# Kernel tuning notes

Measured on AMD Instinct MI355X. Metric: run time of the kernel, lower is better.

The kernel has to match this reference:

```python
import jax, jax.numpy as jnp
import numpy as np

ACT_BITS = 8
W_BITS = 8
C_IN = 64


def round_ste(x):
    # straight-through rounding (Brevitas training behavior)
    return x + jax.lax.stop_gradient(jnp.round(x) - x)


def fake_quant(x, scale, bits, signed):
    if signed:
        lo, hi = -(2 ** (bits - 1)), 2 ** (bits - 1) - 1
    else:
        lo, hi = 0, 2 ** bits - 1
    return jnp.clip(round_ste(x / scale), lo, hi) * scale


def conv_nchw(x, w, pad, groups=1):
    return jax.lax.conv_general_dilated(
        x, w, window_strides=(1, 1), padding=((pad, pad), (pad, pad)),
        dimension_numbers=("NCHW", "OIHW", "NCHW"), feature_group_count=groups)


def setup_inputs() -> dict:
    key = jax.random.key(0)
    k0, k1, k2, k3 = jax.random.split(key, 4)
    x = jax.random.normal(k0, (8, 64, 112, 112), jnp.float32)
    w1 = jax.random.normal(k1, (64, 1, 3, 3), jnp.float32) * 0.05    # depthwise 3x3
    w2 = jax.random.normal(k2, (128, 64, 1, 1), jnp.float32) * 0.05  # pointwise 1x1
    w_sc = jax.random.normal(k3, (128, 64, 1, 1), jnp.float32) * 0.05  # shortcut 1x1
    sc = lambda v: jnp.asarray(v, jnp.float32)
    return dict(x=x, w1=w1, w2=w2, w_sc=w_sc,
                s_in=sc(0.03), s_relu=sc(0.02), s_add=sc(0.03),
                sw1=sc(0.004), sw2=sc(0.004), sw_sc=sc(0.004))


def reference(x, w1, w2, w_sc, s_in, s_relu, s_add, sw1, sw2, sw_sc):
    # quant_input: signed 8-bit fake-quant of the activation
    xq = fake_quant(x, s_in, ACT_BITS, True)
    # shortcut: 1x1 conv with int8 fake-quantized weights (inplane != ouplane)
    identity = conv_nchw(xq, fake_quant(w_sc, sw_sc, W_BITS, True), pad=0)
    # conv1: depthwise 3x3 (groups=inplane) with int8 fake-quantized weights
    y = conv_nchw(xq, fake_quant(w1, sw1, W_BITS, True), pad=1, groups=C_IN)
    # relu2: QuantReLU -> unsigned 8-bit fake-quant of relu
    y = fake_quant(jax.nn.relu(y), s_relu, ACT_BITS, False)
    # conv2: pointwise 1x1
    y = conv_nchw(y, fake_quant(w2, sw2, W_BITS, True), pad=0)
    # residual_add: add then requantize to signed 8-bit
    return fake_quant(y + identity, s_add, ACT_BITS, True)
```

## Files before the change

### kernel.cpp

```cpp
#include <hip/hip_runtime.h>
#include <hip/hip_bf16.h>
#include <stdint.h>

#define NIMG 8
#define CIN  64
#define HWI  12544
#define NP   100352
#define COUT 128

typedef short v8s __attribute__((ext_vector_type(8)));
typedef float v4f __attribute__((ext_vector_type(4)));

static __device__ __forceinline__ int q8(float x, float inv, float lo, float hi) {
    float t = rintf(x * inv);
    t = fminf(fmaxf(t, lo), hi);
    return (int)t;
}

static __device__ __forceinline__ uint32_t funnel(uint32_t hi, uint32_t lo, int sh) {
    return (uint32_t)(((((uint64_t)hi) << 32) | (uint64_t)lo) >> sh);
}

static __device__ __forceinline__ int dot4(uint32_t a, uint32_t b, int c) {
    int acc = c;
    #pragma unroll
    for (int i = 0; i < 4; ++i)
        acc += (int)(int8_t)(a >> (8*i)) * (int)(int8_t)(b >> (8*i));
    return acc;
}

static __device__ __forceinline__ uint16_t i2bf(int v) {
    union { float f; uint32_t u; } c; c.f = (float)v;
    return (uint16_t)(c.u >> 16);
}

__global__ void __launch_bounds__(256) wprep_kernel(
    const float* __restrict__ w2, const float* __restrict__ wsc,
    const float* __restrict__ sw2p, const float* __restrict__ swscp,
    uint16_t* __restrict__ wbuf)
{
    int t = blockIdx.x * 256 + threadIdx.x;
    int f = t * 4;
    int co = f >> 6, k = f & 63;
    float inv2 = 1.0f / sw2p[0];
    float invs = 1.0f / swscp[0];
    float4 a = *(const float4*)(w2 + f);
    float4 b = *(const float4*)(wsc + f);
    float av[4] = {a.x, a.y, a.z, a.w};
    float bv[4] = {b.x, b.y, b.z, b.w};
    uint16_t* d2 = wbuf + co*128 + k;
    uint16_t* ds = wbuf + co*128 + 64 + k;
    *(ushort2*)(d2)     = make_ushort2(i2bf(q8(av[0], inv2, -128.f, 127.f)),
                                       i2bf(q8(av[1], inv2, -128.f, 127.f)));
    *(ushort2*)(d2 + 2) = make_ushort2(i2bf(q8(av[2], inv2, -128.f, 127.f)),
                                       i2bf(q8(av[3], inv2, -128.f, 127.f)));
    *(ushort2*)(ds)     = make_ushort2(i2bf(q8(bv[0], invs, -128.f, 127.f)),
                                       i2bf(q8(bv[1], invs, -128.f, 127.f)));
    *(ushort2*)(ds + 2) = make_ushort2(i2bf(q8(bv[2], invs, -128.f, 127.f)),
                                       i2bf(q8(bv[3], invs, -128.f, 127.f)));
}

__global__ void __launch_bounds__(256) fused_kernel(
    const float* __restrict__ x, const float* __restrict__ w1,
    const uint16_t* __restrict__ wbuf,
    const float* __restrict__ sinp, const float* __restrict__ srelup,
    const float* __restrict__ saddp, const float* __restrict__ sw1p,
    const float* __restrict__ sw2p, const float* __restrict__ swscp,
    float* __restrict__ out)
{
    __shared__ int8_t tile[64 * 468];
    __shared__ int8_t Bl[224 * 132];

    int bid = blockIdx.x;
    int n = bid / 56, ht = bid - n*56, hb = ht*2;
    int tid = threadIdx.x;
    int wave = tid >> 6, lane = tid & 63;
    float sin_f = sinp[0];
    float inv_sin = 1.0f / sin_f;

    for (int i = 0; i < 28; ++i) {
        int id = tid + i*256;
        int c = id / 112; int rem = id - c*112;
        int r = rem / 28; int seg = rem - r*28;
        int grow = hb + r - 1;
        float4 v = make_float4(0.f, 0.f, 0.f, 0.f);
        if ((unsigned)grow < 112u)
            v = *(const float4*)(x + ((size_t)(n*64 + c) * HWI + grow*112 + seg*4));
        float vv[4] = {v.x, v.y, v.z, v.w};
        uint32_t pk = 0;
        #pragma unroll
        for (int e = 0; e < 4; ++e) {
            int q = q8(vv[e], inv_sin, -128.0f, 127.0f);
            pk |= (uint32_t)(q & 255) << (8*e);
        }
        *(uint32_t*)&tile[c*468 + r*116 + seg*4] = pk;
    }
    {
        int c = tid >> 2, r = tid & 3;
        *(uint32_t*)&tile[c*468 + r*116 + 112] = 0;
    }
    __syncthreads();

    {
        int rsel = wave >> 1;
        int half = wave & 1;
        int c = lane;

        float isw1 = 1.0f / sw1p[0];
        uint32_t wp[3];
        #pragma unroll
        for (int ky = 0; ky < 3; ++ky) {
            uint32_t pk = 0;
            #pragma unroll
            for (int kx = 0; kx < 3; ++kx) {
                int q = q8(w1[c*9 + ky*3 + kx], isw1, -128.0f, 127.0f);
                pk |= (uint32_t)(q & 255) << (8*kx);
            }
            wp[ky] = pk;
        }
        float r1 = (sin_f * sw1p[0]) / srelup[0];

        int base[3];
        #pragma unroll
        for (int r2 = 0; r2 < 3; ++r2) base[r2] = c*468 + (rsel + r2)*116;
        int w0b = 56*half;

        uint32_t Ar[3], Br[3], Cr[3];
        #pragma unroll
        for (int r2 = 0; r2 < 3; ++r2) {
            Ar[r2] = half ? *(uint32_t*)&tile[base[r2] + w0b - 4] : 0u;
            Br[r2] = *(uint32_t*)&tile[base[r2] + w0b];
            Cr[r2] = *(uint32_t*)&tile[base[r2] + w0b + 4];
        }

        for (int q = 0; q < 14; ++q) {
            int acc0 = 0, acc1 = 0, acc2 = 0, acc3 = 0;
            #pragma unroll
            for (int r2 = 0; r2 < 3; ++r2) {
                uint32_t d0 = funnel(Br[r2], Ar[r2], 24);
                uint32_t d1 = Br[r2];
                uint32_t d2 = funnel(Cr[r2], Br[r2], 8);
                uint32_t d3 = funnel(Cr[r2], Br[r2], 16);
                acc0 = dot4(d0, wp[r2], acc0);
                acc1 = dot4(d1, wp[r2], acc1);
                acc2 = dot4(d2, wp[r2], acc2);
                acc3 = dot4(d3, wp[r2], acc3);
            }
            int accs[4] = {acc0, acc1, acc2, acc3};
            uint32_t xdw = Br[1];
            int pxb = rsel*112 + w0b + q*4;
            #pragma unroll
            for (int j = 0; j < 4; ++j) {
                float t = rintf((float)accs[j] * r1);
                t = fminf(fmaxf(t, 0.0f), 255.0f);
                Bl[(pxb + j)*132 + c]      = (int8_t)(int)t;
                Bl[(pxb + j)*132 + 64 + c] = (int8_t)((xdw >> (8*j)) & 255);
            }
            #pragma unroll
            for (int r2 = 0; r2 < 3; ++r2) { Ar[r2] = Br[r2]; Br[r2] = Cr[r2]; }
            if (q < 13) {
                #pragma unroll
                for (int r2 = 0; r2 < 3; ++r2)
                    Cr[r2] = *(uint32_t*)&tile[base[r2] + w0b + q*4 + 8];
            }
        }
    }
    __syncthreads();

    {
        int lr = lane >> 4, ln = lane & 15;

        float S2  = sw2p[0] * srelup[0];
        float Ssc = swscp[0] * sinp[0];
        float sadd = saddp[0];
        float inv_sadd = 1.0f / sadd;

        v8s a[2][4];
        #pragma unroll
        for (int mi = 0; mi < 2; ++mi) {
            int m = (wave*2 + mi)*16 + ln;
            #pragma unroll
            for (int seg = 0; seg < 4; ++seg)
                a[mi][seg] = *(const v8s*)(wbuf + (size_t)m*128 + seg*32 + lr*8);
        }

        size_t orow = (size_t)n*COUT*HWI + (size_t)hb*112;

        for (int nt = 0; nt < 14; ++nt) {
            int boff = (nt*16 + ln)*132 + lr*8;
            v8s bf[4];
            #pragma unroll
            for (int seg = 0; seg < 4; ++seg) {
                uint32_t d0 = *(const uint32_t*)&Bl[boff + seg*32];
                uint32_t d1 = *(const uint32_t*)&Bl[boff + seg*32 + 4];
                v8s t;
                if (seg < 2) {
                    #pragma unroll
                    for (int e = 0; e < 4; ++e) {
                        t[e]     = (short)i2bf((int)((d0 >> (8*e)) & 255u));
                        t[4 + e] = (short)i2bf((int)((d1 >> (8*e)) & 255u));
                    }
                } else {
                    #pragma unroll
                    for (int e = 0; e < 4; ++e) {
                        t[e]     = (short)i2bf((int)(int8_t)(d0 >> (8*e)));
                        t[4 + e] = (short)i2bf((int)(int8_t)(d1 >> (8*e)));
                    }
                }
                bf[seg] = t;
            }
            #pragma unroll
            for (int mi = 0; mi < 2; ++mi) {
                v4f acc2 = {0.f, 0.f, 0.f, 0.f};
                v4f accs = {0.f, 0.f, 0.f, 0.f};
                acc2 = __builtin_amdgcn_mfma_f32_16x16x32_bf16(a[mi][0], bf[0], acc2, 0, 0, 0);
                acc2 = __builtin_amdgcn_mfma_f32_16x16x32_bf16(a[mi][1], bf[1], acc2, 0, 0, 0);
                accs = __builtin_amdgcn_mfma_f32_16x16x32_bf16(a[mi][2], bf[2], accs, 0, 0, 0);
                accs = __builtin_amdgcn_mfma_f32_16x16x32_bf16(a[mi][3], bf[3], accs, 0, 0, 0);
                size_t obase = orow + (size_t)((wave*2 + mi)*16 + lr*4)*HWI + nt*16 + ln;
                #pragma unroll
                for (int r = 0; r < 4; ++r) {
                    float v = S2 * acc2[r] + Ssc * accs[r];
                    float t = rintf(v * inv_sadd);
                    t = fminf(fmaxf(t, -128.0f), 127.0f);
                    out[obase + (size_t)r*HWI] = t * sadd;
                }
            }
        }
    }
}

extern "C" void kernel_launch(void* const* d_in, const int* in_sizes, int n_in,
                              void* d_out, int out_size, void* d_ws, size_t ws_size,
                              hipStream_t stream) {
    const float* x     = (const float*)d_in[0];
    const float* w1    = (const float*)d_in[1];
    const float* w2    = (const float*)d_in[2];
    const float* wsc   = (const float*)d_in[3];
    const float* sin   = (const float*)d_in[4];
    const float* srelu = (const float*)d_in[5];
    const float* sadd  = (const float*)d_in[6];
    const float* sw1   = (const float*)d_in[7];
    const float* sw2   = (const float*)d_in[8];
    const float* swsc  = (const float*)d_in[9];

    uint16_t* wbuf = (uint16_t*)d_ws;

    wprep_kernel<<<8, 256, 0, stream>>>(w2, wsc, sw2, swsc, wbuf);
    fused_kernel<<<NIMG * 56, 256, 0, stream>>>(x, w1, wbuf,
                                                sin, srelu, sadd, sw1, sw2, swsc,
                                                (float*)d_out);
}
```

Baseline: 120.9 us.

## Process one output row per block and stage bf16 operands in LDS

Each block now handles a single image row instead of two, which doubles the grid to 896 blocks and reduces the input halo tile from four rows to three. The depthwise stage writes its activations and shortcut inputs to shared memory already converted to bf16, so the MFMA stage loads B fragments with vector reads instead of unpacking bytes. This raises parallelism and cuts ALU work in the GEMM loop. The cost is more halo rereads of x (three rows loaded per output row instead of four per two rows) and a larger bf16 staging buffer.

```diff
diff --git a/kernel.cpp b/kernel.cpp
--- a/kernel.cpp
+++ b/kernel.cpp
@@ -5,7 +5,6 @@
 #define NIMG 8
 #define CIN  64
 #define HWI  12544
-#define NP   100352
 #define COUT 128
 
 typedef short v8s __attribute__((ext_vector_type(8)));
@@ -68,21 +67,22 @@
     const float* __restrict__ sw2p, const float* __restrict__ swscp,
     float* __restrict__ out)
 {
-    __shared__ int8_t tile[64 * 468];
-    __shared__ int8_t Bl[224 * 132];
+    __shared__ int8_t   tile[64 * 348];
+    __shared__ uint16_t Bl[112 * 136];
 
     int bid = blockIdx.x;
-    int n = bid / 56, ht = bid - n*56, hb = ht*2;
+    int n = bid / 112, h = bid - n*112;
     int tid = threadIdx.x;
     int wave = tid >> 6, lane = tid & 63;
+    int lr = lane >> 4, ln = lane & 15;
     float sin_f = sinp[0];
     float inv_sin = 1.0f / sin_f;
 
-    for (int i = 0; i < 28; ++i) {
+    for (int i = 0; i < 21; ++i) {
         int id = tid + i*256;
-        int c = id / 112; int rem = id - c*112;
+        int c = id / 84; int rem = id - c*84;
         int r = rem / 28; int seg = rem - r*28;
-        int grow = hb + r - 1;
+        int grow = h + r - 1;
         float4 v = make_float4(0.f, 0.f, 0.f, 0.f);
         if ((unsigned)grow < 112u)
             v = *(const float4*)(x + ((size_t)(n*64 + c) * HWI + grow*112 + seg*4));
@@ -93,18 +93,17 @@
             int q = q8(vv[e], inv_sin, -128.0f, 127.0f);
             pk |= (uint32_t)(q & 255) << (8*e);
         }
-        *(uint32_t*)&tile[c*468 + r*116 + seg*4] = pk;
-    }
+        *(uint32_t*)&tile[c*348 + r*116 + seg*4] = pk;
+    }
+    if (tid < 192) {
+        int c = tid / 3, r = tid - c*3;
+        *(uint32_t*)&tile[c*348 + r*116 + 112] = 0;
+    }
+    __syncthreads();
+
     {
-        int c = tid >> 2, r = tid & 3;
-        *(uint32_t*)&tile[c*468 + r*116 + 112] = 0;
-    }
-    __syncthreads();
-
-    {
-        int rsel = wave >> 1;
-        int half = wave & 1;
         int c = lane;
+        int w0b = wave * 28;
 
         float isw1 = 1.0f / sw1p[0];
         uint32_t wp[3];
@@ -122,18 +121,17 @@
 
         int base[3];
         #pragma unroll
-        for (int r2 = 0; r2 < 3; ++r2) base[r2] = c*468 + (rsel + r2)*116;
-        int w0b = 56*half;
+        for (int r2 = 0; r2 < 3; ++r2) base[r2] = c*348 + r2*116;
 
         uint32_t Ar[3], Br[3], Cr[3];
         #pragma unroll
         for (int r2 = 0; r2 < 3; ++r2) {
-            Ar[r2] = half ? *(uint32_t*)&tile[base[r2] + w0b - 4] : 0u;
+            Ar[r2] = wave ? *(uint32_t*)&tile[base[r2] + w0b - 4] : 0u;
             Br[r2] = *(uint32_t*)&tile[base[r2] + w0b];
             Cr[r2] = *(uint32_t*)&tile[base[r2] + w0b + 4];
         }
 
-        for (int q = 0; q < 14; ++q) {
+        for (int q = 0; q < 7; ++q) {
             int acc0 = 0, acc1 = 0, acc2 = 0, acc3 = 0;
             #pragma unroll
             for (int r2 = 0; r2 < 3; ++r2) {
@@ -148,17 +146,18 @@
             }
             int accs[4] = {acc0, acc1, acc2, acc3};
             uint32_t xdw = Br[1];
-            int pxb = rsel*112 + w0b + q*4;
+            int pxb = w0b + q*4;
             #pragma unroll
             for (int j = 0; j < 4; ++j) {
                 float t = rintf((float)accs[j] * r1);
                 t = fminf(fmaxf(t, 0.0f), 255.0f);
-                Bl[(pxb + j)*132 + c]      = (int8_t)(int)t;
-                Bl[(pxb + j)*132 + 64 + c] = (int8_t)((xdw >> (8*j)) & 255);
+                int xv = (int)(int8_t)((xdw >> (8*j)) & 255);
+                Bl[(pxb + j)*136 + c]      = i2bf((int)t);
+                Bl[(pxb + j)*136 + 64 + c] = i2bf(xv);
             }
             #pragma unroll
             for (int r2 = 0; r2 < 3; ++r2) { Ar[r2] = Br[r2]; Br[r2] = Cr[r2]; }
-            if (q < 13) {
+            if (q < 6) {
                 #pragma unroll
                 for (int r2 = 0; r2 < 3; ++r2)
                     Cr[r2] = *(uint32_t*)&tile[base[r2] + w0b + q*4 + 8];
@@ -168,8 +167,6 @@
     __syncthreads();
 
     {
-        int lr = lane >> 4, ln = lane & 15;
-
         float S2  = sw2p[0] * srelup[0];
         float Ssc = swscp[0] * sinp[0];
         float sadd = saddp[0];
@@ -184,31 +181,14 @@
                 a[mi][seg] = *(const v8s*)(wbuf + (size_t)m*128 + seg*32 + lr*8);
         }
 
-        size_t orow = (size_t)n*COUT*HWI + (size_t)hb*112;
-
-        for (int nt = 0; nt < 14; ++nt) {
-            int boff = (nt*16 + ln)*132 + lr*8;
+        size_t orow = (size_t)n*COUT*HWI + (size_t)h*112;
+
+        for (int nt = 0; nt < 7; ++nt) {
+            int boff = (nt*16 + ln)*136 + lr*8;
             v8s bf[4];
             #pragma unroll
-            for (int seg = 0; seg < 4; ++seg) {
-                uint32_t d0 = *(const uint32_t*)&Bl[boff + seg*32];
-                uint32_t d1 = *(const uint32_t*)&Bl[boff + seg*32 + 4];
-                v8s t;
-                if (seg < 2) {
-                    #pragma unroll
-                    for (int e = 0; e < 4; ++e) {
-                        t[e]     = (short)i2bf((int)((d0 >> (8*e)) & 255u));
-                        t[4 + e] = (short)i2bf((int)((d1 >> (8*e)) & 255u));
-                    }
-                } else {
-                    #pragma unroll
-                    for (int e = 0; e < 4; ++e) {
-                        t[e]     = (short)i2bf((int)(int8_t)(d0 >> (8*e)));
-                        t[4 + e] = (short)i2bf((int)(int8_t)(d1 >> (8*e)));
-                    }
-                }
-                bf[seg] = t;
-            }
+            for (int seg = 0; seg < 4; ++seg)
+                bf[seg] = *(const v8s*)&Bl[boff + seg*32];
             #pragma unroll
             for (int mi = 0; mi < 2; ++mi) {
                 v4f acc2 = {0.f, 0.f, 0.f, 0.f};
@@ -247,7 +227,7 @@
     uint16_t* wbuf = (uint16_t*)d_ws;
 
     wprep_kernel<<<8, 256, 0, stream>>>(w2, wsc, sw2, swsc, wbuf);
-    fused_kernel<<<NIMG * 56, 256, 0, stream>>>(x, w1, wbuf,
-                                                sin, srelu, sadd, sw1, sw2, swsc,
-                                                (float*)d_out);
-}
+    fused_kernel<<<NIMG * 112, 256, 0, stream>>>(x, w1, wbuf,
+                                                 sin, srelu, sadd, sw1, sw2, swsc,
+                                                 (float*)d_out);
+}
```

Measured after the change: 122.3 us. No clear change (+1.2%).
